# Kernel tuning notes

Hardware: AMD Instinct MI355X
Metric: run time of the kernel (lower is better)

## Reference

```python
import jax
import jax.numpy as jnp
from jax import lax
import numpy as np

IN_SCALE, IN_ZP = 0.01, 7
W_SCALE, W_ZP = 0.01, 3
B_SCALE = 0.0001
I32_MIN, I32_MAX = -(2.0**31), 2.0**31 - 1


def setup_inputs() -> dict:
    key = jax.random.key(0)
    k1, k2, k3 = jax.random.split(key, 3)
    # int8 quantized input activations and weights (torch passes torch.int8 tensors)
    inputVec = jax.random.randint(k1, (32, 128, 56, 56), -128, 128, dtype=jnp.int32).astype(jnp.int8)
    weight = jax.random.randint(k2, (256, 128, 3, 3), -128, 128, dtype=jnp.int32).astype(jnp.int8)
    bias = jax.random.normal(k3, (256,), dtype=jnp.float32)
    return {"inputVec": inputVec, "weight": weight, "bias": bias}


def reference(inputVec, weight, bias):
    # dequantize per-tensor: (q - zero_point) * scale
    x = (inputVec.astype(jnp.float32) - IN_ZP) * IN_SCALE   # [N, Cin, H, W]
    w = (weight.astype(jnp.float32) - W_ZP) * W_SCALE       # [Cout, Cin, kh, kw]
    # quantize bias to qint32 (round-half-even, clamp to int32 range) then dequantize
    b = jnp.clip(jnp.round(bias / B_SCALE), I32_MIN, I32_MAX) * B_SCALE  # [Cout]
    # conv2d: stride 1, no padding, dilation 1, groups 1
    out = lax.conv_general_dilated(
        x, w,
        window_strides=(1, 1),
        padding='VALID',
        dimension_numbers=('NCHW', 'OIHW', 'NCHW'),
    )  # [N, Cout, H-2, W-2]
    return out + b[None, :, None, None]
```

## Files before the change

### kernel.cpp

```cpp
#include <hip/hip_runtime.h>
#include <hip/hip_bf16.h>


#define N_B   32
#define C_IN  128
#define H_IN  56
#define W_IN  56
#define C_OUT 256
#define H_OUT 54
#define W_OUT 54
#define K_TOT 1152
#define NPX   (N_B * H_OUT * W_OUT)
#define PXROW (H_OUT * W_OUT)

using i32x4  = __attribute__((ext_vector_type(4))) int;

static __device__ __forceinline__ int dot4(int a, int b, int c) {
#if __has_builtin(__builtin_amdgcn_sdot4)
  return __builtin_amdgcn_sdot4(a, b, c, false);
#else
  signed char a0 = (signed char)a, a1 = (signed char)(a >> 8),
              a2 = (signed char)(a >> 16), a3 = (signed char)(a >> 24);
  signed char b0 = (signed char)b, b1 = (signed char)(b >> 8),
              b2 = (signed char)(b >> 16), b3 = (signed char)(b >> 24);
  return c + a0 * b0 + a1 * b1 + a2 * b2 + a3 * b3;
#endif
}

__device__ __forceinline__ void gload16(const void* g, void* l) {
  __builtin_amdgcn_global_load_lds(
      (const __attribute__((address_space(1))) void*)g,
      (__attribute__((address_space(3))) void*)l, 16, 0, 0);
}

__global__ void repack_w(const int* __restrict__ w, const float* __restrict__ bias,
                         signed char* __restrict__ wq3, float* __restrict__ bconst) {
  int co = blockIdx.x;
  int ci = threadIdx.x;
  const int* wrow = w + (size_t)co * K_TOT + (size_t)ci * 9;
  int s = 0;
  int kk = ci >> 5, h = (ci >> 4) & 1, b = ci & 15;
  size_t base = (size_t)kk * 8192 + h * 4096 + co * 16 + b;
#pragma unroll
  for (int t = 0; t < 9; ++t) {
    int v = wrow[t];
    s += v;
    wq3[(size_t)t * 32768 + base] = (signed char)v;
  }
  __shared__ int red[128];
  red[ci] = s;
  __syncthreads();
  for (int off = 64; off > 0; off >>= 1) {
    if (ci < off) red[ci] += red[ci + off];
    __syncthreads();
  }
  if (ci == 0) {
    int wsum = red[0];
    float r = rintf(bias[co] / 0.0001f);
    r = fminf(fmaxf(r, -2147483648.0f), 2147483647.0f);
    bconst[co] = 1e-4f * (float)(-7 * wsum + 24192) + r * 0.0001f;
  }
}

__global__ void repack_in(const int* __restrict__ in, signed char* __restrict__ ip2,
                          int* __restrict__ rs) {
  __shared__ int t32[C_IN * W_IN];
  __shared__ int rsum[W_IN];
  int h = blockIdx.x, n = blockIdx.y;
  int tid = threadIdx.x;
  if (tid < W_IN) rsum[tid] = 0;

  int ci = tid >> 1, hf = tid & 1;
  const int* s = in + ((size_t)n * C_IN + ci) * (H_IN * W_IN) + h * W_IN + hf * 28;
  int* d = &t32[ci * W_IN + hf * 28];
#pragma unroll
  for (int k = 0; k < 7; ++k)
    *(int4*)(d + k * 4) = *(const int4*)(s + k * 4);
  __syncthreads();

  signed char* dst = ip2 + ((size_t)n * H_IN + h) * 8192;
#pragma unroll
  for (int jj = 0; jj < 2; ++jj) {
    int j = jj * 256 + tid;
    int q = j >> 6, w = j & 63;
    if (w < W_IN) {
      int b[4], srow = 0;
#pragma unroll
      for (int qq = 0; qq < 4; ++qq) {
        int x0 = t32[(q * 16 + qq * 4 + 0) * W_IN + w];
        int x1 = t32[(q * 16 + qq * 4 + 1) * W_IN + w];
        int x2 = t32[(q * 16 + qq * 4 + 2) * W_IN + w];
        int x3 = t32[(q * 16 + qq * 4 + 3) * W_IN + w];
        b[qq] = (x0 & 255) | ((x1 & 255) << 8) | ((x2 & 255) << 16) | ((x3 & 255) << 24);
        srow = dot4(b[qq], 0x01010101, srow);
      }
      *(int4*)(dst + (size_t)q * 1024 + w * 16) = *(int4*)b;
      atomicAdd(&rsum[w], srow);
    }
  }
  __syncthreads();
  if (tid < W_IN) rs[((size_t)n * H_IN + h) * W_IN + tid] = rsum[tid];
}

__global__ void asum_k(const int* __restrict__ rs, float* __restrict__ asumf) {
  int px = blockIdx.x * 256 + threadIdx.x;
  if (px >= NPX) return;
  int n = px / PXROW, rem = px - n * PXROW;
  int y = rem / W_OUT, x = rem - y * W_OUT;
  const int* rp = rs + ((size_t)n * H_IN + y) * W_IN + x;
  int s = 0;
#pragma unroll
  for (int kh = 0; kh < 3; ++kh)
    s += rp[kh * W_IN + 0] + rp[kh * W_IN + 1] + rp[kh * W_IN + 2];
  asumf[px] = -3e-4f * (float)s;
}

__device__ __forceinline__ int mklb(int pf, int pxl, int c16) {
  int j = pf * 16 + pxl;
  int jc = j > 107 ? 107 : j;
  int dy = (jc >= 54) ? 1 : 0;
  return c16 * 4096 + dy * 1024 + (jc - dy * 54) * 16;
}

__launch_bounds__(256, 5)
__global__ void conv_mfma(const signed char* __restrict__ ip2,
                          const signed char* __restrict__ wq3,
                          const float* __restrict__ asumf,
                          const float* __restrict__ bconst,
                          float* __restrict__ out) {
  __shared__ signed char lds[32768];
  const int tid = threadIdx.x, w = tid >> 6, l = tid & 63;
  const int c16 = l >> 4, pxl = l & 15;

  const int b0 = blockIdx.x;
  const int wg = (b0 & 7) * 432 + (b0 >> 3);
  const int cq = wg & 3;
  const int nr = wg >> 2;
  const int n  = nr / 27;
  const int rp = nr - n * 27;
  const int y0 = rp * 2;

  const signed char* ipn = ip2 + ((size_t)n * H_IN + y0) * 8192;
  {
    const int r = tid >> 6;
    const int off = (tid & 63) * 16;
    const signed char* src = ipn + (size_t)r * 8192 + off;
#pragma unroll
    for (int i = 0; i < 8; ++i)
      gload16(src + (size_t)i * 1024, &lds[i * 4096 + tid * 16]);
  }

  const int lb0 = mklb(0, pxl, c16), lb1 = mklb(1, pxl, c16), lb2 = mklb(2, pxl, c16),
            lb3 = mklb(3, pxl, c16), lb4 = mklb(4, pxl, c16), lb5 = mklb(5, pxl, c16),
            lb6 = mklb(6, pxl, c16);

  const signed char* awq = wq3 + (size_t)c16 * 4096 +
                           (size_t)(cq * 64 + w * 16 + pxl) * 16;

  i32x4 acc0 = {0,0,0,0}, acc1 = {0,0,0,0}, acc2 = {0,0,0,0}, acc3 = {0,0,0,0},
        acc4 = {0,0,0,0}, acc5 = {0,0,0,0}, acc6 = {0,0,0,0};
  i32x4 aX, aY, aZ;

  aX = *(const i32x4*)(awq);
  aY = *(const i32x4*)(awq + 16384);
  __syncthreads();

#define KSTEP(ks, AU, AL, DOLOAD)                                              \
  {                                                                            \
    if (DOLOAD) AL = *(const i32x4*)(awq + (size_t)((ks) + 2) * 16384);        \
    __builtin_amdgcn_sched_barrier(0);                                         \
    constexpr int d_ = ((ks) & 1) * 16384 + (((ks) >> 1) / 3) * 1024 +         \
                       (((ks) >> 1) % 3) * 16;                                 \
    i32x4 q0 = *(const i32x4*)(&lds[lb0 + d_]);                                \
    i32x4 q1 = *(const i32x4*)(&lds[lb1 + d_]);                                \
    i32x4 q2 = *(const i32x4*)(&lds[lb2 + d_]);                                \
    i32x4 q3 = *(const i32x4*)(&lds[lb3 + d_]);                                \
    i32x4 q4 = *(const i32x4*)(&lds[lb4 + d_]);                                \
    i32x4 q5 = *(const i32x4*)(&lds[lb5 + d_]);                                \
    i32x4 q6 = *(const i32x4*)(&lds[lb6 + d_]);                                \
    __builtin_amdgcn_s_setprio(1);                                             \
    acc0 = __builtin_amdgcn_mfma_i32_16x16x64_i8(AU, q0, acc0, 0, 0, 0);       \
    acc1 = __builtin_amdgcn_mfma_i32_16x16x64_i8(AU, q1, acc1, 0, 0, 0);       \
    acc2 = __builtin_amdgcn_mfma_i32_16x16x64_i8(AU, q2, acc2, 0, 0, 0);       \
    acc3 = __builtin_amdgcn_mfma_i32_16x16x64_i8(AU, q3, acc3, 0, 0, 0);       \
    acc4 = __builtin_amdgcn_mfma_i32_16x16x64_i8(AU, q4, acc4, 0, 0, 0);       \
    acc5 = __builtin_amdgcn_mfma_i32_16x16x64_i8(AU, q5, acc5, 0, 0, 0);       \
    acc6 = __builtin_amdgcn_mfma_i32_16x16x64_i8(AU, q6, acc6, 0, 0, 0);       \
    __builtin_amdgcn_s_setprio(0);                                             \
  }

  KSTEP(0,  aX, aZ, 1)  KSTEP(1,  aY, aX, 1)  KSTEP(2,  aZ, aY, 1)
  KSTEP(3,  aX, aZ, 1)  KSTEP(4,  aY, aX, 1)  KSTEP(5,  aZ, aY, 1)
  KSTEP(6,  aX, aZ, 1)  KSTEP(7,  aY, aX, 1)  KSTEP(8,  aZ, aY, 1)
  KSTEP(9,  aX, aZ, 1)  KSTEP(10, aY, aX, 1)  KSTEP(11, aZ, aY, 1)
  KSTEP(12, aX, aZ, 1)  KSTEP(13, aY, aX, 1)  KSTEP(14, aZ, aY, 1)
  KSTEP(15, aX, aZ, 1)  KSTEP(16, aY, aX, 0)  KSTEP(17, aZ, aY, 0)
#undef KSTEP

  float* obase = out + ((size_t)n * C_OUT + cq * 64) * PXROW + y0 * W_OUT;
  const float* apx = asumf + (size_t)n * PXROW + y0 * W_OUT;
  const float asf0 = apx[pxl];
  const float asf1 = apx[16 + pxl];
  const float asf2 = apx[32 + pxl];
  const float asf3 = apx[48 + pxl];
  const float asf4 = apx[64 + pxl];
  const float asf5 = apx[80 + pxl];
  const int j6 = 96 + pxl;
  const float asf6 = (j6 < 108) ? apx[j6] : 0.0f;
#pragma unroll
  for (int j = 0; j < 4; ++j) {
    int co = w * 16 + c16 * 4 + j;
    float bc = bconst[cq * 64 + co];
    float* o = obase + (size_t)co * PXROW;
    o[pxl]      = 1e-4f * (float)acc0[j] + asf0 + bc;
    o[16 + pxl] = 1e-4f * (float)acc1[j] + asf1 + bc;
    o[32 + pxl] = 1e-4f * (float)acc2[j] + asf2 + bc;
    o[48 + pxl] = 1e-4f * (float)acc3[j] + asf3 + bc;
    o[64 + pxl] = 1e-4f * (float)acc4[j] + asf4 + bc;
    o[80 + pxl] = 1e-4f * (float)acc5[j] + asf5 + bc;
    if (j6 < 108)
      o[j6] = 1e-4f * (float)acc6[j] + asf6 + bc;
  }
}

__global__ void conv_naive(const int* __restrict__ in, const int* __restrict__ w,
                           const float* __restrict__ bias, float* __restrict__ out) {
  size_t idx = (size_t)blockIdx.x * 256 + threadIdx.x;
  size_t total = (size_t)N_B * C_OUT * H_OUT * W_OUT;
  if (idx >= total) return;
  int x = idx % W_OUT; size_t t = idx / W_OUT;
  int y = t % H_OUT; t /= H_OUT;
  int co = t % C_OUT; int n = (int)(t / C_OUT);
  int acc = 0;
  for (int ci = 0; ci < C_IN; ++ci) {
    const int* ib = in + (((size_t)n * C_IN + ci) * H_IN + y) * W_IN + x;
    const int* wb = w + (((size_t)co * C_IN + ci) * 3) * 3;
    for (int kh = 0; kh < 3; ++kh)
      for (int kw = 0; kw < 3; ++kw)
        acc += (ib[kh * W_IN + kw] - 7) * (wb[kh * 3 + kw] - 3);
  }
  float r = rintf(bias[co] / 0.0001f);
  r = fminf(fmaxf(r, -2147483648.0f), 2147483647.0f);
  out[idx] = (float)acc * (0.01f * 0.01f) + r * 0.0001f;
}

extern "C" void kernel_launch(void* const* d_in, const int* in_sizes, int n_in,
                              void* d_out, int out_size, void* d_ws, size_t ws_size,
                              hipStream_t stream) {
  const int*   in   = (const int*)d_in[0];
  const int*   w    = (const int*)d_in[1];
  const float* bias = (const float*)d_in[2];
  float*       out  = (float*)d_out;

  const size_t WQ_OFF = 0;
  const size_t IP_OFF = 294912;
  const size_t RS_OFF = IP_OFF + 14680064;
  const size_t AF_OFF = RS_OFF + 401408;
  const size_t BC_OFF = AF_OFF + 373248;
  const size_t NEED   = BC_OFF + 1024;

  if (ws_size >= NEED) {
    char* ws = (char*)d_ws;
    signed char* wq3  = (signed char*)(ws + WQ_OFF);
    signed char* ip2  = (signed char*)(ws + IP_OFF);
    int*         rs   = (int*)(ws + RS_OFF);
    float*       af   = (float*)(ws + AF_OFF);
    float*       bc   = (float*)(ws + BC_OFF);

    repack_w<<<C_OUT, 128, 0, stream>>>(w, bias, wq3, bc);
    repack_in<<<dim3(H_IN, N_B), 256, 0, stream>>>(in, ip2, rs);
    asum_k<<<(NPX + 255) / 256, 256, 0, stream>>>(rs, af);
    conv_mfma<<<3456, 256, 0, stream>>>(ip2, wq3, af, bc, out);
  } else {
    size_t total = (size_t)N_B * C_OUT * H_OUT * W_OUT;
    conv_naive<<<(total + 255) / 256, 256, 0, stream>>>(in, w, bias, out);
  }
}
```

Baseline: 58.49 us.

## Double output channels per block to reuse LDS input tiles across two weight fragments

```diff
diff --git a/kernel.cpp b/kernel.cpp
--- a/kernel.cpp
+++ b/kernel.cpp
@@ -122,7 +122,7 @@
   return c16 * 4096 + dy * 1024 + (jc - dy * 54) * 16;
 }
 
-__launch_bounds__(256, 5)
+__launch_bounds__(256, 4)
 __global__ void conv_mfma(const signed char* __restrict__ ip2,
                           const signed char* __restrict__ wq3,
                           const float* __restrict__ asumf,
@@ -133,9 +133,9 @@
   const int c16 = l >> 4, pxl = l & 15;
 
   const int b0 = blockIdx.x;
-  const int wg = (b0 & 7) * 432 + (b0 >> 3);
-  const int cq = wg & 3;
-  const int nr = wg >> 2;
+  const int wg = (b0 & 7) * 216 + (b0 >> 3);
+  const int cq = wg & 1;
+  const int nr = wg >> 1;
   const int n  = nr / 27;
   const int rp = nr - n * 27;
   const int y0 = rp * 2;
@@ -155,19 +155,24 @@
             lb6 = mklb(6, pxl, c16);
 
   const signed char* awq = wq3 + (size_t)c16 * 4096 +
-                           (size_t)(cq * 64 + w * 16 + pxl) * 16;
-
-  i32x4 acc0 = {0,0,0,0}, acc1 = {0,0,0,0}, acc2 = {0,0,0,0}, acc3 = {0,0,0,0},
-        acc4 = {0,0,0,0}, acc5 = {0,0,0,0}, acc6 = {0,0,0,0};
-  i32x4 aX, aY, aZ;
-
-  aX = *(const i32x4*)(awq);
-  aY = *(const i32x4*)(awq + 16384);
+                           (size_t)(cq * 128 + w * 32 + pxl) * 16;
+
+  i32x4 a0_0 = {0,0,0,0}, a0_1 = {0,0,0,0}, a0_2 = {0,0,0,0}, a0_3 = {0,0,0,0},
+        a0_4 = {0,0,0,0}, a0_5 = {0,0,0,0}, a0_6 = {0,0,0,0};
+  i32x4 a1_0 = {0,0,0,0}, a1_1 = {0,0,0,0}, a1_2 = {0,0,0,0}, a1_3 = {0,0,0,0},
+        a1_4 = {0,0,0,0}, a1_5 = {0,0,0,0}, a1_6 = {0,0,0,0};
+  i32x4 wa0, wa1, wb0, wb1;
+
+#define LDW(P, t)                                                              \
+  P##0 = *(const i32x4*)(awq + (size_t)(t) * 16384);                           \
+  P##1 = *(const i32x4*)(awq + (size_t)(t) * 16384 + 256);
+
+  LDW(wa, 0);
   __syncthreads();
 
-#define KSTEP(ks, AU, AL, DOLOAD)                                              \
+#define KSTEP(ks, U, L, DOLOAD)                                                \
   {                                                                            \
-    if (DOLOAD) AL = *(const i32x4*)(awq + (size_t)((ks) + 2) * 16384);        \
+    if (DOLOAD) { LDW(L, (ks) + 1); }                                          \
     __builtin_amdgcn_sched_barrier(0);                                         \
     constexpr int d_ = ((ks) & 1) * 16384 + (((ks) >> 1) / 3) * 1024 +         \
                        (((ks) >> 1) % 3) * 16;                                 \
@@ -179,25 +184,33 @@
     i32x4 q5 = *(const i32x4*)(&lds[lb5 + d_]);                                \
     i32x4 q6 = *(const i32x4*)(&lds[lb6 + d_]);                                \
     __builtin_amdgcn_s_setprio(1);                                             \
-    acc0 = __builtin_amdgcn_mfma_i32_16x16x64_i8(AU, q0, acc0, 0, 0, 0);       \
-    acc1 = __builtin_amdgcn_mfma_i32_16x16x64_i8(AU, q1, acc1, 0, 0, 0);       \
-    acc2 = __builtin_amdgcn_mfma_i32_16x16x64_i8(AU, q2, acc2, 0, 0, 0);       \
-    acc3 = __builtin_amdgcn_mfma_i32_16x16x64_i8(AU, q3, acc3, 0, 0, 0);       \
-    acc4 = __builtin_amdgcn_mfma_i32_16x16x64_i8(AU, q4, acc4, 0, 0, 0);       \
-    acc5 = __builtin_amdgcn_mfma_i32_16x16x64_i8(AU, q5, acc5, 0, 0, 0);       \
-    acc6 = __builtin_amdgcn_mfma_i32_16x16x64_i8(AU, q6, acc6, 0, 0, 0);       \
+    a0_0 = __builtin_amdgcn_mfma_i32_16x16x64_i8(U##0, q0, a0_0, 0, 0, 0);     \
+    a1_0 = __builtin_amdgcn_mfma_i32_16x16x64_i8(U##1, q0, a1_0, 0, 0, 0);     \
+    a0_1 = __builtin_amdgcn_mfma_i32_16x16x64_i8(U##0, q1, a0_1, 0, 0, 0);     \
+    a1_1 = __builtin_amdgcn_mfma_i32_16x16x64_i8(U##1, q1, a1_1, 0, 0, 0);     \
+    a0_2 = __builtin_amdgcn_mfma_i32_16x16x64_i8(U##0, q2, a0_2, 0, 0, 0);     \
+    a1_2 = __builtin_amdgcn_mfma_i32_16x16x64_i8(U##1, q2, a1_2, 0, 0, 0);     \
+    a0_3 = __builtin_amdgcn_mfma_i32_16x16x64_i8(U##0, q3, a0_3, 0, 0, 0);     \
+    a1_3 = __builtin_amdgcn_mfma_i32_16x16x64_i8(U##1, q3, a1_3, 0, 0, 0);     \
+    a0_4 = __builtin_amdgcn_mfma_i32_16x16x64_i8(U##0, q4, a0_4, 0, 0, 0);     \
+    a1_4 = __builtin_amdgcn_mfma_i32_16x16x64_i8(U##1, q4, a1_4, 0, 0, 0);     \
+    a0_5 = __builtin_amdgcn_mfma_i32_16x16x64_i8(U##0, q5, a0_5, 0, 0, 0);     \
+    a1_5 = __builtin_amdgcn_mfma_i32_16x16x64_i8(U##1, q5, a1_5, 0, 0, 0);     \
+    a0_6 = __builtin_amdgcn_mfma_i32_16x16x64_i8(U##0, q6, a0_6, 0, 0, 0);     \
+    a1_6 = __builtin_amdgcn_mfma_i32_16x16x64_i8(U##1, q6, a1_6, 0, 0, 0);     \
     __builtin_amdgcn_s_setprio(0);                                             \
   }
 
-  KSTEP(0,  aX, aZ, 1)  KSTEP(1,  aY, aX, 1)  KSTEP(2,  aZ, aY, 1)
-  KSTEP(3,  aX, aZ, 1)  KSTEP(4,  aY, aX, 1)  KSTEP(5,  aZ, aY, 1)
-  KSTEP(6,  aX, aZ, 1)  KSTEP(7,  aY, aX, 1)  KSTEP(8,  aZ, aY, 1)
-  KSTEP(9,  aX, aZ, 1)  KSTEP(10, aY, aX, 1)  KSTEP(11, aZ, aY, 1)
-  KSTEP(12, aX, aZ, 1)  KSTEP(13, aY, aX, 1)  KSTEP(14, aZ, aY, 1)
-  KSTEP(15, aX, aZ, 1)  KSTEP(16, aY, aX, 0)  KSTEP(17, aZ, aY, 0)
+  KSTEP(0,  wa, wb, 1)  KSTEP(1,  wb, wa, 1)  KSTEP(2,  wa, wb, 1)
+  KSTEP(3,  wb, wa, 1)  KSTEP(4,  wa, wb, 1)  KSTEP(5,  wb, wa, 1)
+  KSTEP(6,  wa, wb, 1)  KSTEP(7,  wb, wa, 1)  KSTEP(8,  wa, wb, 1)
+  KSTEP(9,  wb, wa, 1)  KSTEP(10, wa, wb, 1)  KSTEP(11, wb, wa, 1)
+  KSTEP(12, wa, wb, 1)  KSTEP(13, wb, wa, 1)  KSTEP(14, wa, wb, 1)
+  KSTEP(15, wb, wa, 1)  KSTEP(16, wa, wb, 1)  KSTEP(17, wb, wa, 0)
 #undef KSTEP
-
-  float* obase = out + ((size_t)n * C_OUT + cq * 64) * PXROW + y0 * W_OUT;
+#undef LDW
+
+  float* obase = out + ((size_t)n * C_OUT + cq * 128) * PXROW + y0 * W_OUT;
   const float* apx = asumf + (size_t)n * PXROW + y0 * W_OUT;
   const float asf0 = apx[pxl];
   const float asf1 = apx[16 + pxl];
@@ -208,18 +221,28 @@
   const int j6 = 96 + pxl;
   const float asf6 = (j6 < 108) ? apx[j6] : 0.0f;
 #pragma unroll
-  for (int j = 0; j < 4; ++j) {
-    int co = w * 16 + c16 * 4 + j;
-    float bc = bconst[cq * 64 + co];
-    float* o = obase + (size_t)co * PXROW;
-    o[pxl]      = 1e-4f * (float)acc0[j] + asf0 + bc;
-    o[16 + pxl] = 1e-4f * (float)acc1[j] + asf1 + bc;
-    o[32 + pxl] = 1e-4f * (float)acc2[j] + asf2 + bc;
-    o[48 + pxl] = 1e-4f * (float)acc3[j] + asf3 + bc;
-    o[64 + pxl] = 1e-4f * (float)acc4[j] + asf4 + bc;
-    o[80 + pxl] = 1e-4f * (float)acc5[j] + asf5 + bc;
-    if (j6 < 108)
-      o[j6] = 1e-4f * (float)acc6[j] + asf6 + bc;
+  for (int m = 0; m < 2; ++m) {
+#pragma unroll
+    for (int j = 0; j < 4; ++j) {
+      int co = w * 32 + m * 16 + c16 * 4 + j;
+      float bc = bconst[cq * 128 + co];
+      float* o = obase + (size_t)co * PXROW;
+      const i32x4& v0 = m ? a1_0 : a0_0;
+      const i32x4& v1 = m ? a1_1 : a0_1;
+      const i32x4& v2 = m ? a1_2 : a0_2;
+      const i32x4& v3 = m ? a1_3 : a0_3;
+      const i32x4& v4 = m ? a1_4 : a0_4;
+      const i32x4& v5 = m ? a1_5 : a0_5;
+      const i32x4& v6 = m ? a1_6 : a0_6;
+      o[pxl]      = 1e-4f * (float)v0[j] + asf0 + bc;
+      o[16 + pxl] = 1e-4f * (float)v1[j] + asf1 + bc;
+      o[32 + pxl] = 1e-4f * (float)v2[j] + asf2 + bc;
+      o[48 + pxl] = 1e-4f * (float)v3[j] + asf3 + bc;
+      o[64 + pxl] = 1e-4f * (float)v4[j] + asf4 + bc;
+      o[80 + pxl] = 1e-4f * (float)v5[j] + asf5 + bc;
+      if (j6 < 108)
+        o[j6] = 1e-4f * (float)v6[j] + asf6 + bc;
+    }
   }
 }
 
@@ -270,7 +293,7 @@
     repack_w<<<C_OUT, 128, 0, stream>>>(w, bias, wq3, bc);
     repack_in<<<dim3(H_IN, N_B), 256, 0, stream>>>(in, ip2, rs);
     asum_k<<<(NPX + 255) / 256, 256, 0, stream>>>(rs, af);
-    conv_mfma<<<3456, 256, 0, stream>>>(ip2, wq3, af, bc, out);
+    conv_mfma<<<1728, 256, 0, stream>>>(ip2, wq3, af, bc, out);
   } else {
     size_t total = (size_t)N_B * C_OUT * H_OUT * W_OUT;
     conv_naive<<<(total + 255) / 256, 256, 0, stream>>>(in, w, bias, out);
```

New measurement: 56.21 us. 3.9% less time.
